# Kernel tuning notes

Measured on AMD Instinct MI355X. Metric: run time of the kernel, lower is better.

Reference implementation:

```python
import jax, jax.numpy as jnp
import numpy as np

N_RBF = 16
N_HIDDEN = 64
CUTOFF = 5.0
N_ATOMS = 4096


def setup_inputs() -> dict:
    key = jax.random.key(0)
    ks = jax.random.split(key, 7)
    # Scale positions so the 5.0 cutoff yields a sparse-ish neighbor graph.
    positions = jax.random.normal(ks[0], (N_ATOMS, 3), dtype=jnp.float32) * 10.0
    s1 = 1.0 / np.sqrt(N_RBF)
    s2 = 1.0 / np.sqrt(N_HIDDEN)
    W1 = jax.random.normal(ks[1], (N_RBF, N_HIDDEN), dtype=jnp.float32) * s1
    b1 = jax.random.normal(ks[2], (N_HIDDEN,), dtype=jnp.float32) * 0.01
    W2 = jax.random.normal(ks[3], (N_HIDDEN, N_HIDDEN), dtype=jnp.float32) * s2
    b2 = jax.random.normal(ks[4], (N_HIDDEN,), dtype=jnp.float32) * 0.01
    W3 = jax.random.normal(ks[5], (N_HIDDEN, 1), dtype=jnp.float32) * s2
    b3 = jax.random.normal(ks[6], (1,), dtype=jnp.float32) * 0.01
    return {"positions": positions, "W1": W1, "b1": b1, "W2": W2, "b2": b2, "W3": W3, "b3": b3}


def _features(positions):
    # positions: (N, 3) -> per-node RBF-aggregated features (N, n_rbf).
    # Equivalent to torch mask.nonzero + scatter_add: features[i] = sum_j in-cutoff rbf(d_ij).
    diff = positions[:, None, :] - positions[None, :, :]          # (N, N, 3)
    dist = jnp.sqrt(jnp.sum(diff * diff, axis=-1))                # (N, N)
    mask = (dist > 1e-6) & (dist < CUTOFF)                        # (N, N)
    centers = jnp.linspace(0.5, CUTOFF, N_RBF, dtype=jnp.float32) # (n_rbf,)
    eta = 0.5 * CUTOFF / N_RBF
    gauss = jnp.exp(-((dist[..., None] - centers) ** 2) / (2.0 * eta * eta))  # (N, N, n_rbf)
    x = jnp.minimum(dist / CUTOFF, 1.0)
    smooth = 0.5 * (1.0 + jnp.cos(jnp.float32(np.pi) * x))        # (N, N)
    w = jnp.where(mask, smooth, 0.0)                              # masked smooth-cutoff weight
    return jnp.einsum('ij,ijk->ik', w, gauss)                     # (N, n_rbf)


def reference(positions, W1, b1, W2, b2, W3, b3):
    feats = _features(positions)                                  # (N, n_rbf)
    h = jax.nn.silu(feats @ W1 + b1)
    h = jax.nn.silu(h @ W2 + b2)
    energy = jnp.sum(h @ W3 + b3)                                 # scalar
    return energy
```

## Files before the change

### kernel.cpp

```cpp
#include <hip/hip_runtime.h>

#define N_ATOMS  4096
#define N_RBF    16
#define N_HIDDEN 64
#define NTHREADS 1024
#define WPB      16
#define APB      16
#define NBLOCKS  (N_ATOMS / APB)
#define QCAP     96
#define QUART    (N_ATOMS / 4)

__device__ __forceinline__ void accum_rbf(float d2, float (&f)[N_RBF]) {
    const float d  = sqrtf(d2);
    const float sm = 0.5f + 0.5f * __cosf(0.62831853071795865f * d);
    #pragma unroll
    for (int k = 0; k < N_RBF; ++k) {
        const float t = d - (0.5f + 0.3f * (float)k);
        f[k] += sm * __expf(-20.48f * t * t);
    }
}

__device__ __forceinline__ int wave_prefix(unsigned long long m) {
    return __builtin_amdgcn_mbcnt_hi((unsigned)(m >> 32),
            __builtin_amdgcn_mbcnt_lo((unsigned)m, 0u));
}

__global__ __launch_bounds__(NTHREADS) void fused_sr_kernel(
    const float* __restrict__ pos,
    const float* __restrict__ W1,
    const float* __restrict__ b1,
    const float* __restrict__ W2,
    const float* __restrict__ b2,
    const float* __restrict__ W3,
    const float* __restrict__ b3,
    float* __restrict__ out,
    float* __restrict__ wsf,
    unsigned* __restrict__ wscnt)
{
    __shared__ __align__(16) float4 sp[N_ATOMS];
    __shared__ __align__(16) float  qd[APB][4][QCAP];
    __shared__ int qcnt[APB][4];
    __shared__ __align__(16) float  h1buf[WPB][N_HIDDEN];
    __shared__ float ered[WPB];

    const int tid = threadIdx.x;

    for (int idx = tid; idx < N_ATOMS; idx += NTHREADS) {
        sp[idx] = make_float4(pos[idx * 3 + 0], pos[idx * 3 + 1], pos[idx * 3 + 2], 0.0f);
    }
    __syncthreads();

    const int lane = tid & 63;
    const int w    = tid >> 6;
    const int t    = w >> 2;
    const int q    = w & 3;
    const int iA   = blockIdx.x * APB + 4 * t;

    const float4 p0 = sp[iA + 0];
    const float4 p1 = sp[iA + 1];
    const float4 p2 = sp[iA + 2];
    const float4 p3 = sp[iA + 3];
    const int jbase = q * QUART;

    int c0_ = 0, c1_ = 0, c2_ = 0, c3_ = 0;

#define PAIR_TEST(P, CNT, AIDX)                                              \
    {                                                                        \
        const float dx = P.x - pj.x, dy = P.y - pj.y, dz = P.z - pj.z;       \
        const float d2 = fmaf(dx, dx, fmaf(dy, dy, dz * dz));                \
        const bool act = (d2 < 25.0f) && (d2 > 1e-12f);                      \
        const unsigned long long m = __ballot(act);                          \
        if (m) {          \
            int widx = CNT + wave_prefix(m);                                 \
            widx = widx < QCAP ? widx : QCAP - 1;                            \
            if (act) qd[4 * t + AIDX][q][widx] = d2;                         \
            CNT += (int)__popcll(m);                                         \
        }                                                                    \
    }

    #pragma unroll 4
    for (int j0 = 0; j0 < QUART; j0 += 64) {
        const float4 pj = sp[jbase + j0 + lane];
        PAIR_TEST(p0, c0_, 0)
        PAIR_TEST(p1, c1_, 1)
        PAIR_TEST(p2, c2_, 2)
        PAIR_TEST(p3, c3_, 3)
    }
#undef PAIR_TEST

    if (lane == 0) {
        qcnt[4 * t + 0][q] = c0_;
        qcnt[4 * t + 1][q] = c1_;
        qcnt[4 * t + 2][q] = c2_;
        qcnt[4 * t + 3][q] = c3_;
    }
    __syncthreads();

    const int co0 = qcnt[w][0], co1 = qcnt[w][1], co2 = qcnt[w][2], co3 = qcnt[w][3];
    const int o1 = co0, o2 = co0 + co1, o3 = o2 + co2, C = o3 + co3;
    float* qrow = &qd[w][0][0];

    float f[N_RBF];
    #pragma unroll
    for (int k = 0; k < N_RBF; ++k) f[k] = 0.0f;
    for (int b = 0; b < C; b += 64) {
        const int g = b + lane;
        const int part = (g >= o1) + (g >= o2) + (g >= o3);
        const int base = part == 0 ? 0 : (part == 1 ? o1 : (part == 2 ? o2 : o3));
        const float d2q = (g < C) ? qrow[part * QCAP + (g - base)] : 1e8f;
        accum_rbf(d2q, f);
    }

    #pragma unroll
    for (int k = 0; k < N_RBF; ++k) {
        f[k] += __shfl_xor(f[k], 32, 64);
        f[k] += __shfl_xor(f[k], 16, 64);
    }
    float* tb = qrow;
    if (lane < 16) {
        #pragma unroll
        for (int j = 0; j < 16; j += 4)
            *reinterpret_cast<float4*>(&tb[lane * 16 + j]) =
                make_float4(f[j], f[j + 1], f[j + 2], f[j + 3]);
    }
    const int kk = lane & 15, rep = lane >> 4;
    float F = 0.0f;
    #pragma unroll
    for (int i = 0; i < 4; ++i) F += tb[(4 * rep + i) * 16 + kk];
    F += __shfl_xor(F, 16, 64);
    F += __shfl_xor(F, 32, 64);
    if (lane < 16) tb[256 + lane] = F;
    float Fb[N_RBF];
    #pragma unroll
    for (int j = 0; j < 16; j += 4) {
        const float4 v = *reinterpret_cast<const float4*>(&tb[256 + j]);
        Fb[j] = v.x; Fb[j + 1] = v.y; Fb[j + 2] = v.z; Fb[j + 3] = v.w;
    }

    float a1 = b1[lane];
    #pragma unroll
    for (int k = 0; k < N_RBF; ++k)
        a1 = fmaf(Fb[k], W1[k * N_HIDDEN + lane], a1);
    const float h1 = a1 / (1.0f + __expf(-a1));

    h1buf[w][lane] = h1;
    float a2 = b2[lane];
    #pragma unroll
    for (int k = 0; k < N_HIDDEN; k += 4) {
        const float4 hv = *reinterpret_cast<const float4*>(&h1buf[w][k]);
        a2 = fmaf(hv.x, W2[(k + 0) * N_HIDDEN + lane], a2);
        a2 = fmaf(hv.y, W2[(k + 1) * N_HIDDEN + lane], a2);
        a2 = fmaf(hv.z, W2[(k + 2) * N_HIDDEN + lane], a2);
        a2 = fmaf(hv.w, W2[(k + 3) * N_HIDDEN + lane], a2);
    }
    const float h2 = a2 / (1.0f + __expf(-a2));

    float e = h2 * W3[lane];
    #pragma unroll
    for (int off = 32; off > 0; off >>= 1)
        e += __shfl_xor(e, off, 64);
    if (lane == 0) ered[w] = e;
    __syncthreads();

    if (w == 0) {
        float acc = (lane < WPB) ? ered[lane] : 0.0f;
        acc += __shfl_xor(acc, 8, 64);
        acc += __shfl_xor(acc, 4, 64);
        acc += __shfl_xor(acc, 2, 64);
        acc += __shfl_xor(acc, 1, 64);
        int last = 0;
        if (lane == 0) {
            wsf[blockIdx.x] = acc + (float)APB * b3[0];
            __threadfence();
            const unsigned old = atomicAdd(wscnt, 1u);
            last = (old == NBLOCKS - 1u) || (old == 0xAAAAAAAAu + (NBLOCKS - 1u));
        }
        last = __shfl(last, 0);
        if (last) {
            __threadfence();
            float tot = wsf[lane] + wsf[lane + 64] + wsf[lane + 128] + wsf[lane + 192];
            #pragma unroll
            for (int off = 32; off > 0; off >>= 1)
                tot += __shfl_xor(tot, off, 64);
            if (lane == 0) out[0] = tot;
        }
    }
}

extern "C" void kernel_launch(void* const* d_in, const int* in_sizes, int n_in,
                              void* d_out, int out_size, void* d_ws, size_t ws_size,
                              hipStream_t stream) {
    const float* pos = (const float*)d_in[0];
    const float* W1  = (const float*)d_in[1];
    const float* b1  = (const float*)d_in[2];
    const float* W2  = (const float*)d_in[3];
    const float* b2  = (const float*)d_in[4];
    const float* W3  = (const float*)d_in[5];
    const float* b3  = (const float*)d_in[6];
    float* out = (float*)d_out;

    float*    wsf   = (float*)d_ws;
    unsigned* wscnt = (unsigned*)((char*)d_ws + NBLOCKS * sizeof(float));

    fused_sr_kernel<<<NBLOCKS, NTHREADS, 0, stream>>>(pos, W1, b1, W2, b2, W3, b3,
                                                      out, wsf, wscnt);
}
```

Before: 80.95 us.

## Split into repack, pair, and finish kernels; read positions from global float4

Adds a repack kernel that converts positions to float4 once, so each block no longer stages all 4096 positions into LDS. The pair kernel now reads neighbor positions straight from global/L2 and uses 512-thread blocks covering 8 atoms, which doubles the block count. The atomic last-block reduction is replaced by a separate one-block finish kernel. The cost is two extra kernel launches and more global loads in the inner loop.

Measured after the change: 80.73 us. No clear change (-0.3%).

```diff
diff --git a/kernel.cpp b/kernel.cpp
--- a/kernel.cpp
+++ b/kernel.cpp
@@ -3,13 +3,20 @@
 #define N_ATOMS  4096
 #define N_RBF    16
 #define N_HIDDEN 64
-#define NTHREADS 1024
-#define WPB      16
-#define APB      16
+#define NTHREADS 512
+#define WPB      8
+#define APB      8
 #define NBLOCKS  (N_ATOMS / APB)
 #define QCAP     96
 #define QUART    (N_ATOMS / 4)
 
+__global__ __launch_bounds__(256) void repack_kernel(const float* __restrict__ pos,
+                                                     float4* __restrict__ pos4) {
+    const int i = blockIdx.x * 256 + threadIdx.x;
+    if (i < N_ATOMS)
+        pos4[i] = make_float4(pos[i * 3 + 0], pos[i * 3 + 1], pos[i * 3 + 2], 0.0f);
+}
+
 __device__ __forceinline__ void accum_rbf(float d2, float (&f)[N_RBF]) {
     const float d  = sqrtf(d2);
     const float sm = 0.5f + 0.5f * __cosf(0.62831853071795865f * d);
@@ -26,40 +33,30 @@
 }
 
 __global__ __launch_bounds__(NTHREADS) void fused_sr_kernel(
-    const float* __restrict__ pos,
+    const float4* __restrict__ pos4,
     const float* __restrict__ W1,
     const float* __restrict__ b1,
     const float* __restrict__ W2,
     const float* __restrict__ b2,
     const float* __restrict__ W3,
-    const float* __restrict__ b3,
-    float* __restrict__ out,
-    float* __restrict__ wsf,
-    unsigned* __restrict__ wscnt)
+    float* __restrict__ partial)
 {
-    __shared__ __align__(16) float4 sp[N_ATOMS];
-    __shared__ __align__(16) float  qd[APB][4][QCAP];
+    __shared__ __align__(16) float qd[APB][4][QCAP];
     __shared__ int qcnt[APB][4];
-    __shared__ __align__(16) float  h1buf[WPB][N_HIDDEN];
+    __shared__ __align__(16) float h1buf[WPB][N_HIDDEN];
     __shared__ float ered[WPB];
 
-    const int tid = threadIdx.x;
-
-    for (int idx = tid; idx < N_ATOMS; idx += NTHREADS) {
-        sp[idx] = make_float4(pos[idx * 3 + 0], pos[idx * 3 + 1], pos[idx * 3 + 2], 0.0f);
-    }
-    __syncthreads();
-
+    const int tid  = threadIdx.x;
     const int lane = tid & 63;
     const int w    = tid >> 6;
     const int t    = w >> 2;
     const int q    = w & 3;
     const int iA   = blockIdx.x * APB + 4 * t;
 
-    const float4 p0 = sp[iA + 0];
-    const float4 p1 = sp[iA + 1];
-    const float4 p2 = sp[iA + 2];
-    const float4 p3 = sp[iA + 3];
+    const float4 p0 = pos4[iA + 0];
+    const float4 p1 = pos4[iA + 1];
+    const float4 p2 = pos4[iA + 2];
+    const float4 p3 = pos4[iA + 3];
     const int jbase = q * QUART;
 
     int c0_ = 0, c1_ = 0, c2_ = 0, c3_ = 0;
@@ -70,7 +67,7 @@
         const float d2 = fmaf(dx, dx, fmaf(dy, dy, dz * dz));                \
         const bool act = (d2 < 25.0f) && (d2 > 1e-12f);                      \
         const unsigned long long m = __ballot(act);                          \
-        if (m) {          \
+        if (m) {                                                             \
             int widx = CNT + wave_prefix(m);                                 \
             widx = widx < QCAP ? widx : QCAP - 1;                            \
             if (act) qd[4 * t + AIDX][q][widx] = d2;                         \
@@ -80,7 +77,7 @@
 
     #pragma unroll 4
     for (int j0 = 0; j0 < QUART; j0 += 64) {
-        const float4 pj = sp[jbase + j0 + lane];
+        const float4 pj = pos4[jbase + j0 + lane];
         PAIR_TEST(p0, c0_, 0)
         PAIR_TEST(p1, c1_, 1)
         PAIR_TEST(p2, c2_, 2)
@@ -162,28 +159,31 @@
     if (lane == 0) ered[w] = e;
     __syncthreads();
 
-    if (w == 0) {
+    if (tid < 64) {
         float acc = (lane < WPB) ? ered[lane] : 0.0f;
-        acc += __shfl_xor(acc, 8, 64);
         acc += __shfl_xor(acc, 4, 64);
         acc += __shfl_xor(acc, 2, 64);
         acc += __shfl_xor(acc, 1, 64);
-        int last = 0;
-        if (lane == 0) {
-            wsf[blockIdx.x] = acc + (float)APB * b3[0];
-            __threadfence();
-            const unsigned old = atomicAdd(wscnt, 1u);
-            last = (old == NBLOCKS - 1u) || (old == 0xAAAAAAAAu + (NBLOCKS - 1u));
-        }
-        last = __shfl(last, 0);
-        if (last) {
-            __threadfence();
-            float tot = wsf[lane] + wsf[lane + 64] + wsf[lane + 128] + wsf[lane + 192];
-            #pragma unroll
-            for (int off = 32; off > 0; off >>= 1)
-                tot += __shfl_xor(tot, off, 64);
-            if (lane == 0) out[0] = tot;
-        }
+        if (lane == 0) partial[blockIdx.x] = acc;
+    }
+}
+
+__global__ __launch_bounds__(NTHREADS) void finish_kernel(
+    const float* __restrict__ partial, const float* __restrict__ b3,
+    float* __restrict__ out) {
+    __shared__ float s[WPB];
+    const int tid = threadIdx.x, lane = tid & 63, w = tid >> 6;
+    float v = partial[tid];
+    #pragma unroll
+    for (int off = 32; off > 0; off >>= 1)
+        v += __shfl_xor(v, off, 64);
+    if (lane == 0) s[w] = v;
+    __syncthreads();
+    if (tid == 0) {
+        float tot = 0.0f;
+        #pragma unroll
+        for (int i = 0; i < WPB; ++i) tot += s[i];
+        out[0] = tot + (float)N_ATOMS * b3[0];
     }
 }
 
@@ -199,9 +199,10 @@
     const float* b3  = (const float*)d_in[6];
     float* out = (float*)d_out;
 
-    float*    wsf   = (float*)d_ws;
-    unsigned* wscnt = (unsigned*)((char*)d_ws + NBLOCKS * sizeof(float));
-
-    fused_sr_kernel<<<NBLOCKS, NTHREADS, 0, stream>>>(pos, W1, b1, W2, b2, W3, b3,
-                                                      out, wsf, wscnt);
-}
+    float4* pos4    = (float4*)d_ws;
+    float*  partial = (float*)((char*)d_ws + N_ATOMS * sizeof(float4));
+
+    repack_kernel<<<(N_ATOMS + 255) / 256, 256, 0, stream>>>(pos, pos4);
+    fused_sr_kernel<<<NBLOCKS, NTHREADS, 0, stream>>>(pos4, W1, b1, W2, b2, W3, partial);
+    finish_kernel<<<1, NTHREADS, 0, stream>>>(partial, b3, out);
+}
```
